# Kernel optimization log

Measured on AMD Instinct MI355X. Metric: run time of the kernel, lower is better.

Reference implementation:

```python
import jax, jax.numpy as jnp
import numpy as np

EPS = 1e-5

def layer_norm(x, w, b):
    mu = jnp.mean(x, axis=-1, keepdims=True)
    var = jnp.mean(jnp.square(x - mu), axis=-1, keepdims=True)
    return (x - mu) * jax.lax.rsqrt(var + EPS) * w + b

def setup_inputs() -> dict:
    key = jax.random.key(0)
    ks = jax.random.split(key, 10)
    B, S, E = 8, 1024, 512
    s = 1.0 / np.sqrt(E)
    return {
        "Zi_1_alpha_beta": jax.random.normal(ks[0], (B, S, E), jnp.float32),
        "Zi_1_alpha": jax.random.normal(ks[1], (B, S, E), jnp.float32),
        "ln_w": jnp.ones((E,), jnp.float32),
        "ln_b": jnp.zeros((E,), jnp.float32),
        "in_proj_w": jax.random.uniform(ks[2], (3 * E, E), jnp.float32, -s, s),
        "in_proj_b": jnp.zeros((3 * E,), jnp.float32),
        "out_proj_w": jax.random.uniform(ks[3], (E, E), jnp.float32, -s, s),
        "out_proj_b": jnp.zeros((E,), jnp.float32),
        "ff_w": jax.random.uniform(ks[4], (E, E), jnp.float32, -s, s),
        "ff_b": jax.random.uniform(ks[5], (E,), jnp.float32, -s, s),
    }

def reference(Zi_1_alpha_beta, Zi_1_alpha, ln_w, ln_b, in_proj_w, in_proj_b,
              out_proj_w, out_proj_b, ff_w, ff_b):
    B, Sq, E = Zi_1_alpha_beta.shape
    Sk = Zi_1_alpha.shape[1]
    H = 8
    dh = E // H

    q_in = layer_norm(Zi_1_alpha_beta, ln_w, ln_b)   # query source
    kv_in = layer_norm(Zi_1_alpha, ln_w, ln_b)       # key/value source

    Wq, Wk, Wv = in_proj_w[:E], in_proj_w[E:2 * E], in_proj_w[2 * E:]
    bq, bk, bv = in_proj_b[:E], in_proj_b[E:2 * E], in_proj_b[2 * E:]
    q = (q_in @ Wq.T + bq).reshape(B, Sq, H, dh)
    k = (kv_in @ Wk.T + bk).reshape(B, Sk, H, dh)
    v = (kv_in @ Wv.T + bv).reshape(B, Sk, H, dh)

    scale = 1.0 / np.sqrt(dh)
    scores = jnp.einsum('bqhd,bkhd->bhqk', q, k) * scale   # [B,H,Sq,Sk]
    attn = jax.nn.softmax(scores, axis=-1)
    ctx = jnp.einsum('bhqk,bkhd->bqhd', attn, v).reshape(B, Sq, E)
    attn_out = ctx @ out_proj_w.T + out_proj_b

    # torch MHA with need_weights=True averages weights over heads
    attn_weights = jnp.mean(attn, axis=1)  # [B,Sq,Sk]

    x = attn_out + Zi_1_alpha_beta
    x_n = layer_norm(x, ln_w, ln_b)
    ff = x_n @ ff_w.T + ff_b
    final = layer_norm(x_n + ff, ln_w, ln_b)
    return final, attn_weights
```

## Files before the change

kernel.cpp:

```cpp
#include <hip/hip_runtime.h>
#include <math.h>

#define EPS 1e-5f

constexpr int B = 8, S = 1024, E = 512, H = 8;
constexpr int M = B * S;

typedef __attribute__((ext_vector_type(8))) short short8;
typedef __attribute__((ext_vector_type(4))) float f32x4;

static __device__ __forceinline__ unsigned short f2bf(float f) {
    unsigned int x = __float_as_uint(f);
    x += 0x7FFFu + ((x >> 16) & 1u);
    return (unsigned short)(x >> 16);
}
static __device__ __forceinline__ float bf2f(unsigned short u) {
    return __uint_as_float(((unsigned int)u) << 16);
}

typedef __attribute__((address_space(3))) unsigned int  lds_uint;
typedef __attribute__((address_space(1))) unsigned int  glb_uint;
static __device__ __forceinline__ void gload16(const unsigned short* g, unsigned short* l) {
    __builtin_amdgcn_global_load_lds((const glb_uint*)g, (lds_uint*)l, 16, 0, 0);
}
template <int N>
static __device__ __forceinline__ void waitvm() {
    __builtin_amdgcn_s_waitcnt(0x0F70 | N);
}

__global__ __launch_bounds__(256) void ln_bf16_kernel(
    const float* __restrict__ x, const float* __restrict__ w,
    const float* __restrict__ bb, unsigned short* __restrict__ out) {
    int row = blockIdx.x * 4 + (threadIdx.x >> 6);
    int lane = threadIdx.x & 63;
    const float* xr = x + (size_t)row * E + lane * 8;
    float4 v0 = *(const float4*)xr;
    float4 v1 = *(const float4*)(xr + 4);
    float vv[8] = {v0.x, v0.y, v0.z, v0.w, v1.x, v1.y, v1.z, v1.w};
    float s = 0.f;
    #pragma unroll
    for (int i = 0; i < 8; i++) s += vv[i];
    #pragma unroll
    for (int o = 1; o < 64; o <<= 1) s += __shfl_xor(s, o);
    float mu = s * (1.0f / E);
    float qs = 0.f;
    #pragma unroll
    for (int i = 0; i < 8; i++) { float d = vv[i] - mu; qs += d * d; }
    #pragma unroll
    for (int o = 1; o < 64; o <<= 1) qs += __shfl_xor(qs, o);
    float rs = rsqrtf(qs * (1.0f / E) + EPS);
    float4 w0 = *(const float4*)(w + lane * 8), w1 = *(const float4*)(w + lane * 8 + 4);
    float4 b0 = *(const float4*)(bb + lane * 8), b1 = *(const float4*)(bb + lane * 8 + 4);
    float ww[8] = {w0.x, w0.y, w0.z, w0.w, w1.x, w1.y, w1.z, w1.w};
    float bv[8] = {b0.x, b0.y, b0.z, b0.w, b1.x, b1.y, b1.z, b1.w};
    short8 o8;
    #pragma unroll
    for (int i = 0; i < 8; i++) o8[i] = (short)f2bf((vv[i] - mu) * rs * ww[i] + bv[i]);
    *(short8*)(out + (size_t)row * E + lane * 8) = o8;
}

__global__ __launch_bounds__(256) void ln_full_kernel(
    const float* __restrict__ x, const float* __restrict__ w,
    const float* __restrict__ bb, float* __restrict__ out) {
    int row = blockIdx.x * 4 + (threadIdx.x >> 6);
    int lane = threadIdx.x & 63;
    const float* xr = x + (size_t)row * E + lane * 8;
    float4 v0 = *(const float4*)xr;
    float4 v1 = *(const float4*)(xr + 4);
    float vv[8] = {v0.x, v0.y, v0.z, v0.w, v1.x, v1.y, v1.z, v1.w};
    float s = 0.f;
    #pragma unroll
    for (int i = 0; i < 8; i++) s += vv[i];
    #pragma unroll
    for (int o = 1; o < 64; o <<= 1) s += __shfl_xor(s, o);
    float mu = s * (1.0f / E);
    float qs = 0.f;
    #pragma unroll
    for (int i = 0; i < 8; i++) { float d = vv[i] - mu; qs += d * d; }
    #pragma unroll
    for (int o = 1; o < 64; o <<= 1) qs += __shfl_xor(qs, o);
    float rs = rsqrtf(qs * (1.0f / E) + EPS);
    float4 w0 = *(const float4*)(w + lane * 8), w1 = *(const float4*)(w + lane * 8 + 4);
    float4 b0 = *(const float4*)(bb + lane * 8), b1 = *(const float4*)(bb + lane * 8 + 4);
    float* op = out + (size_t)row * E + lane * 8;
    float4 o0, o1;
    o0.x = (vv[0] - mu) * rs * w0.x + b0.x;
    o0.y = (vv[1] - mu) * rs * w0.y + b0.y;
    o0.z = (vv[2] - mu) * rs * w0.z + b0.z;
    o0.w = (vv[3] - mu) * rs * w0.w + b0.w;
    o1.x = (vv[4] - mu) * rs * w1.x + b1.x;
    o1.y = (vv[5] - mu) * rs * w1.y + b1.y;
    o1.z = (vv[6] - mu) * rs * w1.z + b1.z;
    o1.w = (vv[7] - mu) * rs * w1.w + b1.w;
    *(float4*)op = o0;
    *(float4*)(op + 4) = o1;
}

__global__ __launch_bounds__(256) void w2bf_kernel(
    const float* __restrict__ wqkv, const float* __restrict__ wo,
    const float* __restrict__ wf, unsigned short* __restrict__ out) {
    int base = (blockIdx.x * 256 + threadIdx.x) * 4;
    float4 v;
    if (base < 3 * E * E)           v = *(const float4*)(wqkv + base);
    else if (base < 4 * E * E)      v = *(const float4*)(wo + (base - 3 * E * E));
    else                            v = *(const float4*)(wf + (base - 4 * E * E));
    ushort4 o;
    o.x = f2bf(v.x); o.y = f2bf(v.y); o.z = f2bf(v.z); o.w = f2bf(v.w);
    *(ushort4*)(out + base) = o;
}

template <int OUT_MODE>
__global__ __launch_bounds__(256) void gemm_mfma(
    const unsigned short* __restrict__ A, const unsigned short* __restrict__ W,
    const float* __restrict__ bias,
    const float* __restrict__ residf, const unsigned short* __restrict__ residb,
    void* __restrict__ C0, void* __restrict__ C1, int Ntot) {
    __shared__ unsigned short As[128 * 32];
    __shared__ unsigned short Bs[128 * 32];
    const int t = threadIdx.x;
    const int wave = t >> 6, lane = t & 63;
    const int quad = lane >> 4, l16 = lane & 15;
    const int m0 = blockIdx.x * 128, n0 = blockIdx.y * 128;
    const int wm = (wave >> 1) * 64, wn = (wave & 1) * 64;

    const int srow = t >> 2;
    const int skof = (t & 3) * 8;

    f32x4 acc[4][4];
    #pragma unroll
    for (int i = 0; i < 4; i++)
        #pragma unroll
        for (int j = 0; j < 4; j++) acc[i][j] = (f32x4){0.f, 0.f, 0.f, 0.f};

    for (int k0 = 0; k0 < E; k0 += 32) {
        gload16(A + (size_t)(m0 + srow) * E + k0 + skof,        As + t * 8);
        gload16(A + (size_t)(m0 + 64 + srow) * E + k0 + skof,   As + 2048 + t * 8);
        gload16(W + (size_t)(n0 + srow) * E + k0 + skof,        Bs + t * 8);
        gload16(W + (size_t)(n0 + 64 + srow) * E + k0 + skof,   Bs + 2048 + t * 8);
        __syncthreads();
        short8 af[4], bfr[4];
        #pragma unroll
        for (int i = 0; i < 4; i++)
            af[i] = *(const short8*)&As[(wm + i * 16 + l16) * 32 + quad * 8];
        #pragma unroll
        for (int j = 0; j < 4; j++)
            bfr[j] = *(const short8*)&Bs[(wn + j * 16 + l16) * 32 + quad * 8];
        #pragma unroll
        for (int i = 0; i < 4; i++)
            #pragma unroll
            for (int j = 0; j < 4; j++)
                acc[i][j] = __builtin_amdgcn_mfma_f32_16x16x32_bf16(af[i], bfr[j], acc[i][j], 0, 0, 0);
        __syncthreads();
    }

    #pragma unroll
    for (int i = 0; i < 4; i++) {
        const int mrow0 = m0 + wm + i * 16 + quad * 4;
        #pragma unroll
        for (int j = 0; j < 4; j++) {
            const int ncol = n0 + wn + j * 16 + l16;
            const float bval = bias[ncol];
            if (OUT_MODE == 0) {
                #pragma unroll
                for (int r = 0; r < 4; r++)
                    ((unsigned short*)C0)[(size_t)(mrow0 + r) * Ntot + ncol] =
                        f2bf(acc[i][j][r] + bval);
            } else if (OUT_MODE == 1) {
                #pragma unroll
                for (int r = 0; r < 4; r++) {
                    size_t idx = (size_t)(mrow0 + r) * Ntot + ncol;
                    ((float*)C0)[idx] = acc[i][j][r] + bval + residf[idx];
                }
            } else if (OUT_MODE == 2) {
                #pragma unroll
                for (int r = 0; r < 4; r++) {
                    size_t idx = (size_t)(mrow0 + r) * Ntot + ncol;
                    ((float*)C0)[idx] = acc[i][j][r] + bval + bf2f(residb[idx]);
                }
            } else {
                if (ncol < 512) {
                    #pragma unroll
                    for (int r = 0; r < 4; r++)
                        ((unsigned short*)C0)[(size_t)(mrow0 + r) * 512 + ncol] =
                            f2bf(acc[i][j][r] + bval);
                } else {
                    const int nv = ncol - 512;
                    const int b2 = mrow0 >> 10, s0v = mrow0 & 1023;
                    ushort4 o;
                    o.x = f2bf(acc[i][j][0] + bval);
                    o.y = f2bf(acc[i][j][1] + bval);
                    o.z = f2bf(acc[i][j][2] + bval);
                    o.w = f2bf(acc[i][j][3] + bval);
                    *(ushort4*)((unsigned short*)C1 + ((size_t)b2 * 512 + nv) * 1024 + s0v) = o;
                }
            }
        }
    }
}

__global__ __launch_bounds__(256, 2) void attn_mfma_kernel(
    const unsigned short* __restrict__ q,
    const unsigned short* __restrict__ k,
    const unsigned short* __restrict__ vt,
    unsigned short* __restrict__ ctx,
    unsigned short* __restrict__ awp) {
    __shared__ unsigned short s_mem[16 * 1032];
    __shared__ unsigned short s_v[4 * 2048];
    __shared__ float s_red[2][4][16];

    const int t = threadIdx.x;
    const int wave = t >> 6, lane = t & 63;
    const int quad = lane >> 4, l16 = lane & 15;
    const int qt   = blockIdx.x & 63;
    const int rest = blockIdx.x >> 6;
    const int hg   = rest & 1;
    const int b    = rest >> 1;
    const int q0   = qt * 16;
    const size_t qrow = ((size_t)(b * S + q0 + l16)) * E;

    unsigned short* karea = s_mem + wave * 4128;
    unsigned short* varea = s_v + wave * 2048;

    const int dr = lane >> 3;
    const int dc = lane & 7;
    const int csrc = dc ^ dr;
    const int sw7 = l16 & 7;

    f32x4 awacc[16];
    #pragma unroll
    for (int i = 0; i < 16; i++) awacc[i] = (f32x4){0.f, 0.f, 0.f, 0.f};

    #pragma clang loop unroll(disable)
    for (int hh = 0; hh < 4; hh++) {
        const int h = hg * 4 + hh;

        auto stage_k = [&](int c, int buf) {
            const unsigned short* src =
                k + ((size_t)(b * S + wave * 256 + c * 32 + dr)) * E + h * 64 + csrc * 8;
            unsigned short* dst = karea + buf * 2048 + dr * 64 + dc * 8;
            gload16(src,                  dst);
            gload16(src + (size_t)8 * E,  dst + 512);
            gload16(src + (size_t)16 * E, dst + 1024);
            gload16(src + (size_t)24 * E, dst + 1536);
        };
        auto stage_v = [&](int cv, int buf) {
            const unsigned short* src =
                vt + ((size_t)(b * E + h * 64 + wave * 16 + dr)) * S + cv * 64 + csrc * 8;
            unsigned short* dst = varea + buf * 1024 + dr * 64 + dc * 8;
            gload16(src,                 dst);
            gload16(src + (size_t)8 * S, dst + 512);
        };

        short8 aq0 = *(const short8*)(q + qrow + h * 64 + quad * 8);
        short8 aq1 = *(const short8*)(q + qrow + h * 64 + 32 + quad * 8);

        f32x4 sacc[16];
        stage_k(0, 0);
        stage_k(1, 1);
        #pragma unroll
        for (int c = 0; c < 8; c++) {
            if (c < 7) waitvm<4>(); else waitvm<0>();
            const unsigned short* kbuf = karea + (c & 1) * 2048;
            #pragma unroll
            for (int ntl = 0; ntl < 2; ntl++) {
                const int rl = ntl * 16 + l16;
                short8 kf0 = *(const short8*)(kbuf + rl * 64 + ((quad)     ^ sw7) * 8);
                short8 kf1 = *(const short8*)(kbuf + rl * 64 + ((4 + quad) ^ sw7) * 8);
                f32x4 cc = (f32x4){0.f, 0.f, 0.f, 0.f};
                cc = __builtin_amdgcn_mfma_f32_16x16x32_bf16(aq0, kf0, cc, 0, 0, 0);
                cc = __builtin_amdgcn_mfma_f32_16x16x32_bf16(aq1, kf1, cc, 0, 0, 0);
                sacc[c * 2 + ntl] = cc * 0.125f;
            }
            if (c < 6) stage_k(c + 2, c & 1);
        }

        float lm[4], ls[4];
        #pragma unroll
        for (int r = 0; r < 4; r++) {
            float mv = sacc[0][r];
            #pragma unroll
            for (int nt = 1; nt < 16; nt++) mv = fmaxf(mv, sacc[nt][r]);
            #pragma unroll
            for (int o = 1; o < 16; o <<= 1) mv = fmaxf(mv, __shfl_xor(mv, o));
            lm[r] = mv;
            ls[r] = 0.f;
        }
        #pragma unroll
        for (int nt = 0; nt < 16; nt++)
            #pragma unroll
            for (int r = 0; r < 4; r++) {
                float e = __expf(sacc[nt][r] - lm[r]);
                sacc[nt][r] = e;
                ls[r] += e;
            }
        #pragma unroll
        for (int r = 0; r < 4; r++) {
            #pragma unroll
            for (int o = 1; o < 16; o <<= 1) ls[r] += __shfl_xor(ls[r], o);
        }
        if (l16 == 0) {
            #pragma unroll
            for (int r = 0; r < 4; r++) {
                s_red[0][wave][quad * 4 + r] = lm[r];
                s_red[1][wave][quad * 4 + r] = ls[r];
            }
        }
        __syncthreads();
        float scale[4];
        #pragma unroll
        for (int r = 0; r < 4; r++) {
            const int row = quad * 4 + r;
            float m0 = s_red[0][0][row], m1 = s_red[0][1][row];
            float m2 = s_red[0][2][row], m3 = s_red[0][3][row];
            float gmax = fmaxf(fmaxf(m0, m1), fmaxf(m2, m3));
            float gsum = s_red[1][0][row] * __expf(m0 - gmax)
                       + s_red[1][1][row] * __expf(m1 - gmax)
                       + s_red[1][2][row] * __expf(m2 - gmax)
                       + s_red[1][3][row] * __expf(m3 - gmax);
            scale[r] = __expf(lm[r] - gmax) / gsum;
        }

        #pragma unroll
        for (int nt = 0; nt < 16; nt++) {
            #pragma unroll
            for (int r = 0; r < 4; r++) {
                float p = sacc[nt][r] * scale[r];
                awacc[nt][r] += p;
                s_mem[(quad * 4 + r) * 1032 + wave * 256 + nt * 16 + l16] = f2bf(p);
            }
        }
        __syncthreads();

        f32x4 cacc0 = (f32x4){0.f, 0.f, 0.f, 0.f};
        f32x4 cacc1 = (f32x4){0.f, 0.f, 0.f, 0.f};
        stage_v(0, 0);
        stage_v(1, 1);
        #pragma unroll
        for (int cv = 0; cv < 16; cv++) {
            if (cv < 15) waitvm<2>(); else waitvm<0>();
            const unsigned short* vbuf = varea + (cv & 1) * 1024;
            short8 vf0 = *(const short8*)(vbuf + l16 * 64 + ((quad)     ^ sw7) * 8);
            short8 vf1 = *(const short8*)(vbuf + l16 * 64 + ((4 + quad) ^ sw7) * 8);
            short8 pf0 = *(const short8*)(s_mem + l16 * 1032 + cv * 64 + quad * 8);
            short8 pf1 = *(const short8*)(s_mem + l16 * 1032 + cv * 64 + 32 + quad * 8);
            cacc0 = __builtin_amdgcn_mfma_f32_16x16x32_bf16(pf0, vf0, cacc0, 0, 0, 0);
            cacc1 = __builtin_amdgcn_mfma_f32_16x16x32_bf16(pf1, vf1, cacc1, 0, 0, 0);
            if (cv < 14) stage_v(cv + 2, cv & 1);
        }
        f32x4 cacc = cacc0 + cacc1;
        unsigned short* crow = ctx + ((size_t)(b * S + q0)) * E + h * 64 + wave * 16 + l16;
        #pragma unroll
        for (int r = 0; r < 4; r++)
            crow[(size_t)(quad * 4 + r) * E] = f2bf(cacc[r]);
        __syncthreads();
    }

    #pragma unroll
    for (int nt = 0; nt < 16; nt++) {
        #pragma unroll
        for (int r = 0; r < 4; r++)
            awp[((size_t)((hg * B + b) * S + q0 + quad * 4 + r)) * S +
                wave * 256 + nt * 16 + l16] = f2bf(awacc[nt][r]);
    }
}

template <int NP>
__global__ __launch_bounds__(256) void aw_reduce_kernel(
    const unsigned short* __restrict__ awp, float* __restrict__ aw) {
    const size_t PLN = (size_t)B * S * S;
    size_t idx = ((size_t)blockIdx.x * 256 + threadIdx.x) * 8;
    float acc[8] = {};
    #pragma unroll
    for (int p = 0; p < NP; p++) {
        short8 v = *(const short8*)(awp + p * PLN + idx);
        #pragma unroll
        for (int j = 0; j < 8; j++) acc[j] += bf2f((unsigned short)v[j]);
    }
    float4 o0 = make_float4(acc[0] * (1.0f / H), acc[1] * (1.0f / H),
                            acc[2] * (1.0f / H), acc[3] * (1.0f / H));
    float4 o1 = make_float4(acc[4] * (1.0f / H), acc[5] * (1.0f / H),
                            acc[6] * (1.0f / H), acc[7] * (1.0f / H));
    *(float4*)(aw + idx) = o0;
    *(float4*)(aw + idx + 4) = o1;
}

extern "C" void kernel_launch(void* const* d_in, const int* in_sizes, int n_in,
                              void* d_out, int out_size, void* d_ws, size_t ws_size,
                              hipStream_t stream) {
    const float* Zab  = (const float*)d_in[0];
    const float* Za   = (const float*)d_in[1];
    const float* lnw  = (const float*)d_in[2];
    const float* lnb  = (const float*)d_in[3];
    const float* Wqkv = (const float*)d_in[4];
    const float* bqkv = (const float*)d_in[5];
    const float* Wo   = (const float*)d_in[6];
    const float* bo   = (const float*)d_in[7];
    const float* Wf   = (const float*)d_in[8];
    const float* bf   = (const float*)d_in[9];

    float* out_final = (float*)d_out;
    float* out_aw    = out_final + (size_t)B * S * E;

    char* ws = (char*)d_ws;
    unsigned short* qb   = (unsigned short*)(ws);
    unsigned short* kb   = (unsigned short*)(ws + (8u << 20));
    unsigned short* vtb  = (unsigned short*)(ws + (16u << 20));
    unsigned short* ctxb = (unsigned short*)(ws + (24u << 20));
    unsigned short* aqb  = (unsigned short*)(ws + (32u << 20));
    unsigned short* akvb = (unsigned short*)(ws + (40u << 20));
    unsigned short* awp  = (unsigned short*)(ws + (32ull << 20));
    unsigned short* wbf  = (unsigned short*)(ws + (96ull << 20));
    float* xb  = (float*)(ws);
    float* tb  = (float*)(ws + (16u << 20));
    unsigned short* xnb = aqb;

    dim3 blk(256);

    w2bf_kernel<<<(5 * E * E) / 1024, blk, 0, stream>>>(Wqkv, Wo, Wf, wbf);

    ln_bf16_kernel<<<M / 4, blk, 0, stream>>>(Zab, lnw, lnb, aqb);
    ln_bf16_kernel<<<M / 4, blk, 0, stream>>>(Za,  lnw, lnb, akvb);

    gemm_mfma<0><<<dim3(M / 128, 4), blk, 0, stream>>>(aqb,  wbf,               bqkv,     nullptr, nullptr, qb, nullptr, 512);
    gemm_mfma<3><<<dim3(M / 128, 8), blk, 0, stream>>>(akvb, wbf + (size_t)E*E, bqkv + E, nullptr, nullptr, kb, vtb, 1024);

    attn_mfma_kernel<<<B * 2 * 64, blk, 0, stream>>>(qb, kb, vtb, ctxb, awp);
    aw_reduce_kernel<2><<<4096, blk, 0, stream>>>(awp, out_aw);

    gemm_mfma<1><<<dim3(M / 128, 4), blk, 0, stream>>>(ctxb, wbf + (size_t)3*E*E, bo, Zab, nullptr, xb, nullptr, 512);

    ln_bf16_kernel<<<M / 4, blk, 0, stream>>>(xb, lnw, lnb, xnb);

    gemm_mfma<2><<<dim3(M / 128, 4), blk, 0, stream>>>(xnb, wbf + (size_t)4*E*E, bf, nullptr, xnb, tb, nullptr, 512);

    ln_full_kernel<<<M / 4, blk, 0, stream>>>(tb, lnw, lnb, out_final);
}
```

Before: 277.4 us.

## Merge Q and KV projection GEMMs and load V fragments directly from global

The separate Q and KV projection launches are combined into one gemm_qkv kernel with a 12-wide grid, giving one larger launch. In attention, V is no longer staged through LDS with async copies. Each lane now reads its V^T fragments straight from global memory into registers, double-buffered. Dropping the V shared buffer frees LDS, so launch bounds rise to 4 blocks per CU, trading async-copy latency hiding for occupancy and possibly more register pressure.

```diff
diff --git a/kernel.cpp b/kernel.cpp
--- a/kernel.cpp
+++ b/kernel.cpp
@@ -114,7 +114,7 @@
     const unsigned short* __restrict__ A, const unsigned short* __restrict__ W,
     const float* __restrict__ bias,
     const float* __restrict__ residf, const unsigned short* __restrict__ residb,
-    void* __restrict__ C0, void* __restrict__ C1, int Ntot) {
+    void* __restrict__ C0, int Ntot) {
     __shared__ unsigned short As[128 * 32];
     __shared__ unsigned short Bs[128 * 32];
     const int t = threadIdx.x;
@@ -160,52 +160,109 @@
         for (int j = 0; j < 4; j++) {
             const int ncol = n0 + wn + j * 16 + l16;
             const float bval = bias[ncol];
-            if (OUT_MODE == 0) {
-                #pragma unroll
-                for (int r = 0; r < 4; r++)
-                    ((unsigned short*)C0)[(size_t)(mrow0 + r) * Ntot + ncol] =
-                        f2bf(acc[i][j][r] + bval);
-            } else if (OUT_MODE == 1) {
+            if (OUT_MODE == 1) {
                 #pragma unroll
                 for (int r = 0; r < 4; r++) {
                     size_t idx = (size_t)(mrow0 + r) * Ntot + ncol;
                     ((float*)C0)[idx] = acc[i][j][r] + bval + residf[idx];
                 }
-            } else if (OUT_MODE == 2) {
+            } else {
                 #pragma unroll
                 for (int r = 0; r < 4; r++) {
                     size_t idx = (size_t)(mrow0 + r) * Ntot + ncol;
                     ((float*)C0)[idx] = acc[i][j][r] + bval + bf2f(residb[idx]);
                 }
+            }
+        }
+    }
+}
+
+__global__ __launch_bounds__(256) void gemm_qkv(
+    const unsigned short* __restrict__ Aq, const unsigned short* __restrict__ Akv,
+    const unsigned short* __restrict__ W,
+    const float* __restrict__ bias,
+    unsigned short* __restrict__ qout,
+    unsigned short* __restrict__ kout,
+    unsigned short* __restrict__ vtout) {
+    __shared__ unsigned short As[128 * 32];
+    __shared__ unsigned short Bs[128 * 32];
+    const int t = threadIdx.x;
+    const int wave = t >> 6, lane = t & 63;
+    const int quad = lane >> 4, l16 = lane & 15;
+    const bool isq = blockIdx.y < 4;
+    const int yy = isq ? blockIdx.y : blockIdx.y - 4;
+    const unsigned short* A  = isq ? Aq : Akv;
+    const unsigned short* Wb = W + (isq ? 0 : (size_t)E * E);
+    const float* bb = bias + (isq ? 0 : E);
+    const int m0 = blockIdx.x * 128, n0 = yy * 128;
+    const int wm = (wave >> 1) * 64, wn = (wave & 1) * 64;
+
+    const int srow = t >> 2;
+    const int skof = (t & 3) * 8;
+
+    f32x4 acc[4][4];
+    #pragma unroll
+    for (int i = 0; i < 4; i++)
+        #pragma unroll
+        for (int j = 0; j < 4; j++) acc[i][j] = (f32x4){0.f, 0.f, 0.f, 0.f};
+
+    for (int k0 = 0; k0 < E; k0 += 32) {
+        gload16(A + (size_t)(m0 + srow) * E + k0 + skof,         As + t * 8);
+        gload16(A + (size_t)(m0 + 64 + srow) * E + k0 + skof,    As + 2048 + t * 8);
+        gload16(Wb + (size_t)(n0 + srow) * E + k0 + skof,        Bs + t * 8);
+        gload16(Wb + (size_t)(n0 + 64 + srow) * E + k0 + skof,   Bs + 2048 + t * 8);
+        __syncthreads();
+        short8 af[4], bfr[4];
+        #pragma unroll
+        for (int i = 0; i < 4; i++)
+            af[i] = *(const short8*)&As[(wm + i * 16 + l16) * 32 + quad * 8];
+        #pragma unroll
+        for (int j = 0; j < 4; j++)
+            bfr[j] = *(const short8*)&Bs[(wn + j * 16 + l16) * 32 + quad * 8];
+        #pragma unroll
+        for (int i = 0; i < 4; i++)
+            #pragma unroll
+            for (int j = 0; j < 4; j++)
+                acc[i][j] = __builtin_amdgcn_mfma_f32_16x16x32_bf16(af[i], bfr[j], acc[i][j], 0, 0, 0);
+        __syncthreads();
+    }
+
+    #pragma unroll
+    for (int i = 0; i < 4; i++) {
+        const int mrow0 = m0 + wm + i * 16 + quad * 4;
+        #pragma unroll
+        for (int j = 0; j < 4; j++) {
+            const int ncol = n0 + wn + j * 16 + l16;
+            const float bval = bb[ncol];
+            if (isq) {
+                #pragma unroll
+                for (int r = 0; r < 4; r++)
+                    qout[(size_t)(mrow0 + r) * 512 + ncol] = f2bf(acc[i][j][r] + bval);
+            } else if (ncol < 512) {
+                #pragma unroll
+                for (int r = 0; r < 4; r++)
+                    kout[(size_t)(mrow0 + r) * 512 + ncol] = f2bf(acc[i][j][r] + bval);
             } else {
-                if (ncol < 512) {
-                    #pragma unroll
-                    for (int r = 0; r < 4; r++)
-                        ((unsigned short*)C0)[(size_t)(mrow0 + r) * 512 + ncol] =
-                            f2bf(acc[i][j][r] + bval);
-                } else {
-                    const int nv = ncol - 512;
-                    const int b2 = mrow0 >> 10, s0v = mrow0 & 1023;
-                    ushort4 o;
-                    o.x = f2bf(acc[i][j][0] + bval);
-                    o.y = f2bf(acc[i][j][1] + bval);
-                    o.z = f2bf(acc[i][j][2] + bval);
-                    o.w = f2bf(acc[i][j][3] + bval);
-                    *(ushort4*)((unsigned short*)C1 + ((size_t)b2 * 512 + nv) * 1024 + s0v) = o;
-                }
-            }
-        }
-    }
-}
-
-__global__ __launch_bounds__(256, 2) void attn_mfma_kernel(
+                const int nv = ncol - 512;
+                const int b2 = mrow0 >> 10, s0v = mrow0 & 1023;
+                ushort4 o;
+                o.x = f2bf(acc[i][j][0] + bval);
+                o.y = f2bf(acc[i][j][1] + bval);
+                o.z = f2bf(acc[i][j][2] + bval);
+                o.w = f2bf(acc[i][j][3] + bval);
+                *(ushort4*)(vtout + ((size_t)b2 * 512 + nv) * 1024 + s0v) = o;
+            }
+        }
+    }
+}
+
+__global__ __launch_bounds__(256, 4) void attn_mfma_kernel(
     const unsigned short* __restrict__ q,
     const unsigned short* __restrict__ k,
     const unsigned short* __restrict__ vt,
     unsigned short* __restrict__ ctx,
     unsigned short* __restrict__ awp) {
     __shared__ unsigned short s_mem[16 * 1032];
-    __shared__ unsigned short s_v[4 * 2048];
     __shared__ float s_red[2][4][16];
 
     const int t = threadIdx.x;
@@ -219,7 +276,6 @@
     const size_t qrow = ((size_t)(b * S + q0 + l16)) * E;
 
     unsigned short* karea = s_mem + wave * 4128;
-    unsigned short* varea = s_v + wave * 2048;
 
     const int dr = lane >> 3;
     const int dc = lane & 7;
@@ -242,13 +298,6 @@
             gload16(src + (size_t)8 * E,  dst + 512);
             gload16(src + (size_t)16 * E, dst + 1024);
             gload16(src + (size_t)24 * E, dst + 1536);
-        };
-        auto stage_v = [&](int cv, int buf) {
-            const unsigned short* src =
-                vt + ((size_t)(b * E + h * 64 + wave * 16 + dr)) * S + cv * 64 + csrc * 8;
-            unsigned short* dst = varea + buf * 1024 + dr * 64 + dc * 8;
-            gload16(src,                 dst);
-            gload16(src + (size_t)8 * S, dst + 512);
         };
 
         short8 aq0 = *(const short8*)(q + qrow + h * 64 + quad * 8);
@@ -331,21 +380,26 @@
         }
         __syncthreads();
 
+        const unsigned short* vbase =
+            vt + ((size_t)(b * E + h * 64 + wave * 16 + l16)) * S + quad * 8;
         f32x4 cacc0 = (f32x4){0.f, 0.f, 0.f, 0.f};
         f32x4 cacc1 = (f32x4){0.f, 0.f, 0.f, 0.f};
-        stage_v(0, 0);
-        stage_v(1, 1);
+        short8 va[2], vb[2];
+        #pragma unroll
+        for (int cv = 0; cv < 2; cv++) {
+            va[cv] = *(const short8*)(vbase + cv * 64);
+            vb[cv] = *(const short8*)(vbase + cv * 64 + 32);
+        }
         #pragma unroll
         for (int cv = 0; cv < 16; cv++) {
-            if (cv < 15) waitvm<2>(); else waitvm<0>();
-            const unsigned short* vbuf = varea + (cv & 1) * 1024;
-            short8 vf0 = *(const short8*)(vbuf + l16 * 64 + ((quad)     ^ sw7) * 8);
-            short8 vf1 = *(const short8*)(vbuf + l16 * 64 + ((4 + quad) ^ sw7) * 8);
             short8 pf0 = *(const short8*)(s_mem + l16 * 1032 + cv * 64 + quad * 8);
             short8 pf1 = *(const short8*)(s_mem + l16 * 1032 + cv * 64 + 32 + quad * 8);
-            cacc0 = __builtin_amdgcn_mfma_f32_16x16x32_bf16(pf0, vf0, cacc0, 0, 0, 0);
-            cacc1 = __builtin_amdgcn_mfma_f32_16x16x32_bf16(pf1, vf1, cacc1, 0, 0, 0);
-            if (cv < 14) stage_v(cv + 2, cv & 1);
+            cacc0 = __builtin_amdgcn_mfma_f32_16x16x32_bf16(pf0, va[cv & 1], cacc0, 0, 0, 0);
+            cacc1 = __builtin_amdgcn_mfma_f32_16x16x32_bf16(pf1, vb[cv & 1], cacc1, 0, 0, 0);
+            if (cv < 14) {
+                va[cv & 1] = *(const short8*)(vbase + (cv + 2) * 64);
+                vb[cv & 1] = *(const short8*)(vbase + (cv + 2) * 64 + 32);
+            }
         }
         f32x4 cacc = cacc0 + cacc1;
         unsigned short* crow = ctx + ((size_t)(b * S + q0)) * E + h * 64 + wave * 16 + l16;
@@ -421,17 +475,16 @@
     ln_bf16_kernel<<<M / 4, blk, 0, stream>>>(Zab, lnw, lnb, aqb);
     ln_bf16_kernel<<<M / 4, blk, 0, stream>>>(Za,  lnw, lnb, akvb);
 
-    gemm_mfma<0><<<dim3(M / 128, 4), blk, 0, stream>>>(aqb,  wbf,               bqkv,     nullptr, nullptr, qb, nullptr, 512);
-    gemm_mfma<3><<<dim3(M / 128, 8), blk, 0, stream>>>(akvb, wbf + (size_t)E*E, bqkv + E, nullptr, nullptr, kb, vtb, 1024);
+    gemm_qkv<<<dim3(M / 128, 12), blk, 0, stream>>>(aqb, akvb, wbf, bqkv, qb, kb, vtb);
 
     attn_mfma_kernel<<<B * 2 * 64, blk, 0, stream>>>(qb, kb, vtb, ctxb, awp);
     aw_reduce_kernel<2><<<4096, blk, 0, stream>>>(awp, out_aw);
 
-    gemm_mfma<1><<<dim3(M / 128, 4), blk, 0, stream>>>(ctxb, wbf + (size_t)3*E*E, bo, Zab, nullptr, xb, nullptr, 512);
+    gemm_mfma<1><<<dim3(M / 128, 4), blk, 0, stream>>>(ctxb, wbf + (size_t)3*E*E, bo, Zab, nullptr, xb, 512);
 
     ln_bf16_kernel<<<M / 4, blk, 0, stream>>>(xb, lnw, lnb, xnb);
 
-    gemm_mfma<2><<<dim3(M / 128, 4), blk, 0, stream>>>(xnb, wbf + (size_t)4*E*E, bf, nullptr, xnb, tb, nullptr, 512);
+    gemm_mfma<2><<<dim3(M / 128, 4), blk, 0, stream>>>(xnb, wbf + (size_t)4*E*E, bf, nullptr, xnb, tb, 512);
 
     ln_full_kernel<<<M / 4, blk, 0, stream>>>(tb, lnw, lnb, out_final);
 }
```

New measurement: 345.6 us. 1.25x slower.
